# Optimization experiments

Hardware: AMD Instinct MI355X
Metric: run time of the kernel (lower is better)

## Reference

```python
import jax, jax.numpy as jnp
import numpy as np

ATT_DIM = 512
HEADS = 8
HEAD_DIM = ATT_DIM // HEADS
D_IN = 512
LEFT_MASK = 256
RIGHT_MASK = 0
LARGE = 1e30


def pos_encoding(S, d):
    # Transformer-XL sinusoid table over relative positions S-1 .. -(S-1), length 2S-1.
    inv_freq = (1.0 / (10000.0 ** (np.arange(0, d, 2.0) / d))).astype(np.float32)
    pos = jnp.arange(S - 1, -S, -1, dtype=jnp.float32)          # [2S-1]
    ang = pos[:, None] * jnp.asarray(inv_freq)[None, :]          # [2S-1, d/2]
    # concat([sin, cos], -1) on a trailing singleton -> interleaved sin/cos per frequency
    return jnp.stack([jnp.sin(ang), jnp.cos(ang)], axis=-1).reshape(2 * S - 1, d)


def rel_shift(x):
    # x: [B, N, S, 2S-1] -> [B, N, S, S] with out[i, j] = x[i, S-1 - i + j]
    B, N, S, L = x.shape
    x = jnp.pad(x, ((0, 0), (0, 0), (0, 0), (1, 0)))             # [B,N,S,L+1]
    x = x.reshape(B, N, L + 1, S)[:, :, 1:, :]                   # [B,N,L,S]
    x = x.reshape(B, N, S, L)
    return x[:, :, :, :S]


def setup_inputs() -> dict:
    key = jax.random.key(0)
    ks = jax.random.split(key, 9)
    B, S, D = 2, 2048, D_IN
    scale = 0.02
    return {
        "x": jax.random.normal(ks[0], (B, S, D), dtype=jnp.float32),
        "Wq": jax.random.normal(ks[1], (D, ATT_DIM), dtype=jnp.float32) * scale,
        "b_con": jax.random.normal(ks[2], (ATT_DIM,), dtype=jnp.float32) * scale,
        "b_rel": jax.random.normal(ks[3], (ATT_DIM,), dtype=jnp.float32) * scale,
        "Wk": jax.random.normal(ks[4], (D, ATT_DIM), dtype=jnp.float32) * scale,
        "Wkr": jax.random.normal(ks[5], (D_IN, ATT_DIM), dtype=jnp.float32) * scale,
        "Wv": jax.random.normal(ks[6], (D, ATT_DIM), dtype=jnp.float32) * scale,
        "bv": jax.random.normal(ks[7], (ATT_DIM,), dtype=jnp.float32) * scale,
        "x_len": jax.random.randint(ks[8], (B,), 1, S + 1).astype(jnp.int32),
    }


def reference(x, Wq, b_con, b_rel, Wk, Wkr, Wv, bv, x_len):
    B, S, D = x.shape
    N, Dh = HEADS, HEAD_DIM

    # content/relative query share the kernel (TiedDense) with separate biases
    q_lin = jnp.einsum('bsd,de->bse', x, Wq)
    q_con = (q_lin + b_con).reshape(B, S, N, Dh)
    q_rel = (q_lin + b_rel).reshape(B, S, N, Dh)
    k_con = jnp.einsum('bsd,de->bse', x, Wk).reshape(B, S, N, Dh)

    content_energy = jnp.einsum('bind,bjnd->bnij', q_con, k_con)  # [B,N,S,S]

    pos_emb = pos_encoding(S, D_IN)                               # [2S-1, D]
    k_rel = (pos_emb @ Wkr).reshape(2 * S - 1, N, Dh)
    relative_energy = jnp.einsum('bind,jnd->bnij', q_rel, k_rel)  # [B,N,S,2S-1]
    relative_energy = rel_shift(relative_energy)                  # [B,N,S,S]

    energy = (content_energy + relative_energy) / jnp.sqrt(jnp.float32(Dh))

    # sequence mask over keys (broadcast [B,1,1,S]) * banded mask (band_part)
    j = jnp.arange(S)
    seq_mask = (j[None, :] < x_len[:, None]).astype(jnp.float32)[:, None, None, :]
    i = jnp.arange(S)[:, None]
    band = ((i - j[None, :] <= LEFT_MASK) & (j[None, :] - i <= RIGHT_MASK)).astype(jnp.float32)
    mask = seq_mask * band[None, None, :, :]

    masked_energy = energy - (1.0 - mask) * LARGE
    attention = jax.nn.softmax(masked_energy, axis=-1)

    v = (jnp.einsum('bsd,de->bse', x, Wv) + bv).reshape(B, S, N, Dh)
    context = jnp.einsum('bnij,bjnd->bind', attention, v).reshape(B, S, N * Dh)
    return context
```

## Files before the change

### kernel.cpp

```cpp
#include <hip/hip_runtime.h>
#include <math.h>

#define S_ 2048
#define NH 8
#define CSL 320
#define LP 72

typedef __attribute__((ext_vector_type(8))) short short8;
typedef __attribute__((ext_vector_type(4))) float f32x4;
typedef unsigned short ushort_t;

__device__ __forceinline__ short bf16r(float x) {
    union { float f; unsigned u; } v; v.f = x;
    unsigned r = v.u + 0x7fffu + ((v.u >> 16) & 1u);
    return (short)(r >> 16);
}
__device__ __forceinline__ float b2f(ushort_t h) {
    union { float f; unsigned u; } v; v.u = ((unsigned)h) << 16; return v.f;
}

__global__ __launch_bounds__(256) void prep_kernel(
    const float* __restrict__ x,
    const float* __restrict__ Wq, const float* __restrict__ Wk,
    const float* __restrict__ Wv, const float* __restrict__ Wkr,
    ushort_t* __restrict__ WTq, ushort_t* __restrict__ WTk,
    ushort_t* __restrict__ WTv, ushort_t* __restrict__ WTkr,
    ushort_t* __restrict__ pos, ushort_t* __restrict__ xb16)
{
    const int widx = blockIdx.z;
    const int t = threadIdx.x;
    if (widx == 4) {
        const int base = blockIdx.y * 8 + blockIdx.x;
        const float C = -0.051905126482615036f;
        const int f = t;
#pragma unroll
        for (int rep = 0; rep < 6; ++rep) {
            const int r = base + rep * 64;
            unsigned pk = 0;
            if (r <= 256) {
                float ang = (float)r * exp2f(C * (float)f);
                unsigned s = (unsigned)(ushort_t)bf16r(sinf(ang));
                unsigned c = (unsigned)(ushort_t)bf16r(cosf(ang));
                pk = s | (c << 16);
            }
            ((unsigned*)pos)[(size_t)r * 256 + f] = pk;
        }
        return;
    }
    if (widx == 5) {
        const int sub = blockIdx.y * 8 + blockIdx.x;
        const size_t base = (size_t)sub * 32768;
#pragma unroll
        for (int it = 0; it < 8; ++it) {
            const size_t idx = base + (size_t)it * 4096 + (size_t)t * 16;
            const float* src = &x[idx];
            ushort_t t16[16];
#pragma unroll
            for (int u = 0; u < 16; ++u) t16[u] = (ushort_t)bf16r(src[u]);
            *(short8*)&xb16[idx]     = *(short8*)&t16[0];
            *(short8*)&xb16[idx + 8] = *(short8*)&t16[8];
        }
        return;
    }
    const float* W = (widx == 0) ? Wq : (widx == 1) ? Wk : (widx == 2) ? Wv : Wkr;
    ushort_t* WT   = (widx == 0) ? WTq : (widx == 1) ? WTk : (widx == 2) ? WTv : WTkr;
    const int k0 = blockIdx.x * 64, n0 = blockIdx.y * 64;
    __shared__ __align__(16) ushort_t T[64][72];
    const int srow = t >> 2, sc0 = (t & 3) * 16;
    const float* src = &W[(size_t)(k0 + srow) * 512 + n0 + sc0];
#pragma unroll
    for (int u = 0; u < 16; ++u) T[sc0 + u][srow] = (ushort_t)bf16r(src[u]);
    __syncthreads();
    ushort_t* dst = &WT[(size_t)(n0 + srow) * 512 + k0 + sc0];
    *(short8*)dst       = *(const short8*)&T[srow][sc0];
    *(short8*)(dst + 8) = *(const short8*)&T[srow][sc0 + 8];
}

__global__ __launch_bounds__(256) void qkv_gemm(
    const ushort_t* __restrict__ xb16,
    const ushort_t* __restrict__ WTq, const ushort_t* __restrict__ WTk,
    const ushort_t* __restrict__ WTv,
    const ushort_t* __restrict__ pos, const ushort_t* __restrict__ WTkr,
    const float* __restrict__ b_con, const float* __restrict__ b_rel,
    const float* __restrict__ bv, const int* __restrict__ xlen_p,
    ushort_t* __restrict__ qcon, ushort_t* __restrict__ qrel,
    ushort_t* __restrict__ kout, ushort_t* __restrict__ vT,
    ushort_t* __restrict__ krel)
{
    const int widx = blockIdx.y >> 3;
    const int tid = threadIdx.x, lane = tid & 63, w = tid >> 6;
    const int quad = lane >> 4, l16 = lane & 15;

    __shared__ __align__(16) ushort_t A_lds[2][128][40];
    __shared__ __align__(16) ushort_t B_lds[2][64][40];

    f32x4 acc[2][4];
#pragma unroll
    for (int mt = 0; mt < 2; ++mt)
#pragma unroll
        for (int nt = 0; nt < 4; ++nt) acc[mt][nt] = (f32x4){0.f, 0.f, 0.f, 0.f};

    const int arow = tid >> 1, ak0 = (tid & 1) * 16;
    const int brow = tid >> 2, bk0 = (tid & 3) * 8;

    const ushort_t* Asrc;
    const ushort_t* Bsrc;

    if (widx < 2) {
        const int m0 = blockIdx.x * 128;
        {
            const int xl = xlen_p[m0 >> 11];
            const int s0 = m0 & 2047;
            if (widx == 0) { if (s0 >= xl + 256) return; }
            else           { if (s0 >= xl + 63)  return; }
        }
        const int n0 = (blockIdx.y & 7) * 64;
        const ushort_t* WT = (widx == 0) ? WTq : WTk;
        Asrc = &xb16[(size_t)(m0 + arow) * 512 + ak0];
        Bsrc = &WT[(size_t)(n0 + brow) * 512 + bk0];
    } else if (widx == 2) {
        const int vb = (blockIdx.y & 7) * 32 + blockIdx.x;
        const int m0d = (vb & 3) * 128;
        const int n0j = (vb >> 2) * 64;
        Asrc = &WTv[(size_t)(m0d + arow) * 512 + ak0];
        Bsrc = &xb16[(size_t)(n0j + brow) * 512 + bk0];
    } else {
        if (blockIdx.x >= 24) return;
        const int m0 = (blockIdx.x >> 3) * 128;
        const int n0 = (blockIdx.x & 7) * 64;
        Asrc = &pos[(size_t)(m0 + arow) * 512 + ak0];
        Bsrc = &WTkr[(size_t)(n0 + brow) * 512 + bk0];
    }

    {
        short8 pa0 = *(const short8*)Asrc;
        short8 pa1 = *(const short8*)(Asrc + 8);
        short8 pb  = *(const short8*)Bsrc;
        *(short8*)&A_lds[0][arow][ak0]     = pa0;
        *(short8*)&A_lds[0][arow][ak0 + 8] = pa1;
        *(short8*)&B_lds[0][brow][bk0]     = pb;
        pa0 = *(const short8*)(Asrc + 32);
        pa1 = *(const short8*)(Asrc + 40);
        pb  = *(const short8*)(Bsrc + 32);
        __syncthreads();

#pragma unroll 1
        for (int it = 0; it < 16; ++it) {
            const int cur = it & 1;
            if (it < 15) {
                *(short8*)&A_lds[cur ^ 1][arow][ak0]     = pa0;
                *(short8*)&A_lds[cur ^ 1][arow][ak0 + 8] = pa1;
                *(short8*)&B_lds[cur ^ 1][brow][bk0]     = pb;
                if (it < 14) {
                    pa0 = *(const short8*)(Asrc + it * 32 + 64);
                    pa1 = *(const short8*)(Asrc + it * 32 + 72);
                    pb  = *(const short8*)(Bsrc + it * 32 + 64);
                }
            }
            short8 a0 = *(const short8*)&A_lds[cur][w * 32 + l16][quad * 8];
            short8 a1 = *(const short8*)&A_lds[cur][w * 32 + 16 + l16][quad * 8];
#pragma unroll
            for (int nt = 0; nt < 4; ++nt) {
                short8 bb = *(const short8*)&B_lds[cur][nt * 16 + l16][quad * 8];
                acc[0][nt] = __builtin_amdgcn_mfma_f32_16x16x32_bf16(a0, bb, acc[0][nt], 0, 0, 0);
                acc[1][nt] = __builtin_amdgcn_mfma_f32_16x16x32_bf16(a1, bb, acc[1][nt], 0, 0, 0);
            }
            __syncthreads();
        }
    }

    if (widx < 2) {
        const int m0 = blockIdx.x * 128;
        const int n0 = (blockIdx.y & 7) * 64;
#pragma unroll
        for (int nt = 0; nt < 4; ++nt) {
            const int col = n0 + nt * 16 + l16;
            float bc = 0.f, br = 0.f;
            if (widx == 0) { bc = b_con[col]; br = b_rel[col]; }
#pragma unroll
            for (int mt = 0; mt < 2; ++mt) {
#pragma unroll
                for (int reg = 0; reg < 4; ++reg) {
                    const size_t m = (size_t)(m0 + w * 32 + mt * 16 + quad * 4 + reg);
                    const float val = acc[mt][nt][reg];
                    if (widx == 0) {
                        qcon[m * 512 + col] = (ushort_t)bf16r((val + bc) * 0.125f);
                        qrel[m * 512 + col] = (ushort_t)bf16r((val + br) * 0.125f);
                    } else {
                        kout[m * 512 + col] = (ushort_t)bf16r(val);
                    }
                }
            }
        }
    } else if (widx == 2) {
        const int vb = (blockIdx.y & 7) * 32 + blockIdx.x;
        const int m0d = (vb & 3) * 128;
        const int n0j = (vb >> 2) * 64;
        const int b = n0j >> 11;
#pragma unroll
        for (int mt = 0; mt < 2; ++mt) {
#pragma unroll
            for (int reg = 0; reg < 4; ++reg) {
                const int d = m0d + w * 32 + mt * 16 + quad * 4 + reg;
                const int n = d >> 6, dd = d & 63;
                const float bvv = bv[d];
#pragma unroll
                for (int nt = 0; nt < 4; ++nt) {
                    const int s = (n0j + nt * 16 + l16) & 2047;
                    vT[((size_t)((b * NH + n) * 64 + dd)) * 2048 + s] =
                        (ushort_t)bf16r(acc[mt][nt][reg] + bvv);
                }
            }
        }
    } else {
        const int m0 = (blockIdx.x >> 3) * 128;
        const int n0 = (blockIdx.x & 7) * 64;
#pragma unroll
        for (int nt = 0; nt < 4; ++nt) {
            const int col = n0 + nt * 16 + l16;
#pragma unroll
            for (int mt = 0; mt < 2; ++mt)
#pragma unroll
                for (int reg = 0; reg < 4; ++reg) {
                    const size_t m = (size_t)(m0 + w * 32 + mt * 16 + quad * 4 + reg);
                    krel[m * 512 + col] = (ushort_t)bf16r(acc[mt][nt][reg]);
                }
        }
    }
}

__global__ __launch_bounds__(256) void rel_gemm(
    const ushort_t* __restrict__ qrel, const ushort_t* __restrict__ krel,
    const ushort_t* __restrict__ vT, const int* __restrict__ xlen_p,
    ushort_t* __restrict__ R3, float* __restrict__ vmean)
{
    const int tile = blockIdx.x, n = blockIdx.y, b = blockIdx.z;
    const int tid = threadIdx.x, lane = tid & 63, w = tid >> 6;
    const int quad = lane >> 4, l16 = lane & 15;

    __shared__ __align__(16) ushort_t A_lds[128][LP];
    __shared__ __align__(16) ushort_t B_lds[2][64][LP];

    if (tile == 16) {
        const int row = tid >> 2, seg = tid & 3;
        const ushort_t* src = &vT[((size_t)((b * NH + n) * 64 + row)) * 2048 + seg * 512];
        float sum = 0.f;
        for (int it = 0; it < 64; ++it) {
            short8 h = *(const short8*)(src + it * 8);
#pragma unroll
            for (int u = 0; u < 8; ++u) sum += b2f((ushort_t)h[u]);
        }
        float* scratch = (float*)A_lds;
        scratch[row * 4 + seg] = sum;
        __syncthreads();
        if (tid < 64) {
            float s = scratch[tid * 4] + scratch[tid * 4 + 1]
                    + scratch[tid * 4 + 2] + scratch[tid * 4 + 3];
            vmean[(size_t)b * 512 + n * 64 + tid] = s * (1.0f / (float)S_);
        }
        return;
    }

    const int i0 = tile * 128;
    if (i0 >= xlen_p[b] + 256) return;

    {
        const int srow = tid >> 1, sc0 = (tid & 1) * 32;
        const ushort_t* src = &qrel[((size_t)b * S_ + i0 + srow) * 512 + n * 64 + sc0];
#pragma unroll
        for (int u = 0; u < 4; ++u)
            *(short8*)&A_lds[srow][sc0 + u * 8] = *(const short8*)(src + u * 8);
    }

    const size_t rbase3 = (size_t)(b * NH + n) * S_ * CSL;
    const int srow2 = tid >> 2, sc2 = (tid & 3) * 16;

    short8 pb0, pb1;
    auto issueB = [&](int rc) {
        const ushort_t* src = &krel[(size_t)(rc * 64 + srow2) * 512 + n * 64 + sc2];
        pb0 = *(const short8*)src;
        pb1 = *(const short8*)(src + 8);
    };
    issueB(0);
    *(short8*)&B_lds[0][srow2][sc2]     = pb0;
    *(short8*)&B_lds[0][srow2][sc2 + 8] = pb1;
    issueB(1);
    __syncthreads();

#pragma unroll 1
    for (int rc = 0; rc < 5; ++rc) {
        const int cur = rc & 1;
        if (rc < 4) {
            *(short8*)&B_lds[cur ^ 1][srow2][sc2]     = pb0;
            *(short8*)&B_lds[cur ^ 1][srow2][sc2 + 8] = pb1;
            if (rc < 3) issueB(rc + 2);
        }

        short8 a[2][2];
#pragma unroll
        for (int mt = 0; mt < 2; ++mt) {
            a[mt][0] = *(const short8*)&A_lds[w * 32 + mt * 16 + l16][quad * 8];
            a[mt][1] = *(const short8*)&A_lds[w * 32 + mt * 16 + l16][quad * 8 + 32];
        }
#pragma unroll
        for (int nt = 0; nt < 4; ++nt) {
            short8 b0 = *(const short8*)&B_lds[cur][nt * 16 + l16][quad * 8];
            short8 b1 = *(const short8*)&B_lds[cur][nt * 16 + l16][quad * 8 + 32];
            const int r = rc * 64 + nt * 16 + l16;
#pragma unroll
            for (int mt = 0; mt < 2; ++mt) {
                f32x4 s = (f32x4){0.f, 0.f, 0.f, 0.f};
                s = __builtin_amdgcn_mfma_f32_16x16x32_bf16(a[mt][0], b0, s, 0, 0, 0);
                s = __builtin_amdgcn_mfma_f32_16x16x32_bf16(a[mt][1], b1, s, 0, 0, 0);
                if (r <= 256) {
#pragma unroll
                    for (int reg = 0; reg < 4; ++reg) {
                        const int ig = i0 + w * 32 + mt * 16 + quad * 4 + reg;
                        const int cslot = (ig & 63) + 256 - r;
                        R3[rbase3 + (size_t)ig * CSL + cslot] = (ushort_t)bf16r(s[reg]);
                    }
                }
            }
        }
        __syncthreads();
    }
}

__global__ __launch_bounds__(256) void attn_kernel(
    const ushort_t* __restrict__ qcon, const ushort_t* __restrict__ kbuf,
    const ushort_t* __restrict__ vT, const ushort_t* __restrict__ R3,
    const float* __restrict__ vmean, const int* __restrict__ xlen_p,
    float* __restrict__ out)
{
    const int bx = blockIdx.x;
    const int tile = ((bx & 7) << 2) | (bx >> 3);
    const int n = blockIdx.y, b = blockIdx.z;
    const int i0 = tile * 64;
    const int tid = threadIdx.x, lane = tid & 63, w = tid >> 6;
    const int quad = lane >> 4, l16 = lane & 15;
    const int xlen = xlen_p[b];

    if (i0 >= xlen + 256) {
        const int row = tid >> 2, cf = (tid & 3) * 16;
        const float* vm = &vmean[(size_t)b * 512 + n * 64 + cf];
        float* dst = &out[((size_t)b * S_ + i0 + row) * 512 + n * 64 + cf];
#pragma unroll
        for (int u = 0; u < 16; u += 4)
            *(float4*)&dst[u] = *(const float4*)&vm[u];
        return;
    }
    int nchunk = (xlen - i0 + 256 + 63) >> 6;
    if (nchunk > 5) nchunk = 5;
    const int c0 = (i0 < 256) ? ((256 - i0) >> 6) : 0;

    __shared__ __align__(16) ushort_t k_lds[64][LP];
    __shared__ __align__(16) ushort_t vT_lds[64][LP];
    __shared__ __align__(16) ushort_t Rl_lds[64][LP];

    const ushort_t* qc = &qcon[((size_t)b * S_ + i0 + w * 16 + l16) * 512 + n * 64 + quad * 8];
    const short8 aq0 = *(const short8*)qc;
    const short8 aq1 = *(const short8*)(qc + 32);

    f32x4 Oa[4];
#pragma unroll
    for (int nt = 0; nt < 4; ++nt) Oa[nt] = (f32x4){0.f, 0.f, 0.f, 0.f};
    float lpart[4] = {};

    const size_t rbase3 = (size_t)(b * NH + n) * S_ * CSL;
    const size_t vTbase = (size_t)((b * NH + n) * 64) * 2048;
    const int srow = tid >> 2, sc0 = (tid & 3) * 16;

    short8 kr[2], vr[2], rr[2], kn[2], vn[2], rn[2];

    auto issue = [&](int c, short8* kd, short8* vd, short8* rd) {
        const int jc0 = i0 - 256 + c * 64;
        const ushort_t* ks = &kbuf[((size_t)b * S_ + jc0 + srow) * 512 + n * 64 + sc0];
        kd[0] = *(const short8*)ks;
        kd[1] = *(const short8*)(ks + 8);
        const ushort_t* vs = &vT[vTbase + (size_t)srow * 2048 + jc0 + sc0];
        vd[0] = *(const short8*)vs;
        vd[1] = *(const short8*)(vs + 8);
        const ushort_t* Rs = &R3[rbase3 + (size_t)(i0 + srow) * CSL + c * 64 + sc0];
        rd[0] = *(const short8*)Rs;
        rd[1] = *(const short8*)(Rs + 8);
    };

    issue(c0, kr, vr, rr);

#pragma unroll 1
    for (int c = c0; c < nchunk; ++c) {
        const int jc0 = i0 - 256 + c * 64;
        __syncthreads();
        *(short8*)&k_lds[srow][sc0]      = kr[0];
        *(short8*)&k_lds[srow][sc0 + 8]  = kr[1];
        *(short8*)&vT_lds[srow][sc0]     = vr[0];
        *(short8*)&vT_lds[srow][sc0 + 8] = vr[1];
        *(short8*)&Rl_lds[srow][sc0]     = rr[0];
        *(short8*)&Rl_lds[srow][sc0 + 8] = rr[1];
        if (c + 1 < nchunk) issue(c + 1, kn, vn, rn);
        __syncthreads();

        f32x4 Sacc[4];
#pragma unroll
        for (int jt = 0; jt < 4; ++jt) {
            short8 bk0 = *(const short8*)&k_lds[jt * 16 + l16][quad * 8];
            short8 bk1 = *(const short8*)&k_lds[jt * 16 + l16][quad * 8 + 32];
            f32x4 s = (f32x4){0.f, 0.f, 0.f, 0.f};
            s = __builtin_amdgcn_mfma_f32_16x16x32_bf16(aq0, bk0, s, 0, 0, 0);
            s = __builtin_amdgcn_mfma_f32_16x16x32_bf16(aq1, bk1, s, 0, 0, 0);
            Sacc[jt] = s;
        }

#pragma unroll
        for (int jt = 0; jt < 4; ++jt) {
#pragma unroll
            for (int reg = 0; reg < 4; ++reg) {
                const int row = w * 16 + quad * 4 + reg;
                const int i = i0 + row;
                const int j = jc0 + jt * 16 + l16;
                const int r = i - j;
                const bool valid = (j < xlen) && (r >= 0) && (r <= 256);
                float rvv = b2f(Rl_lds[row][jt * 16 + l16]);
                float e = valid ? __expf(Sacc[jt][reg] + rvv) : 0.f;
                lpart[reg] += e;
                Rl_lds[row][jt * 16 + l16] = (ushort_t)bf16r(e);
            }
        }

        short8 ap0 = *(const short8*)&Rl_lds[w * 16 + l16][quad * 8];
        short8 ap1 = *(const short8*)&Rl_lds[w * 16 + l16][quad * 8 + 32];
#pragma unroll
        for (int nt = 0; nt < 4; ++nt) {
            short8 bv0 = *(const short8*)&vT_lds[nt * 16 + l16][quad * 8];
            short8 bv1 = *(const short8*)&vT_lds[nt * 16 + l16][quad * 8 + 32];
            Oa[nt] = __builtin_amdgcn_mfma_f32_16x16x32_bf16(ap0, bv0, Oa[nt], 0, 0, 0);
            Oa[nt] = __builtin_amdgcn_mfma_f32_16x16x32_bf16(ap1, bv1, Oa[nt], 0, 0, 0);
        }

        kr[0] = kn[0]; kr[1] = kn[1];
        vr[0] = vn[0]; vr[1] = vn[1];
        rr[0] = rn[0]; rr[1] = rn[1];
    }

#pragma unroll
    for (int reg = 0; reg < 4; ++reg) {
#pragma unroll
        for (int off = 1; off < 16; off <<= 1)
            lpart[reg] += __shfl_xor(lpart[reg], off, 64);
    }

#pragma unroll
    for (int reg = 0; reg < 4; ++reg) {
        const int i = i0 + w * 16 + quad * 4 + reg;
        const bool dead = (i >= xlen + 256);
        const float linv = 1.0f / lpart[reg];
#pragma unroll
        for (int nt = 0; nt < 4; ++nt) {
            const int d = n * 64 + nt * 16 + l16;
            float val = dead ? vmean[(size_t)b * 512 + d] : Oa[nt][reg] * linv;
            out[((size_t)b * S_ + i) * 512 + d] = val;
        }
    }
}

extern "C" void kernel_launch(void* const* d_in, const int* in_sizes, int n_in,
                              void* d_out, int out_size, void* d_ws, size_t ws_size,
                              hipStream_t stream) {
    const float* x     = (const float*)d_in[0];
    const float* Wq    = (const float*)d_in[1];
    const float* b_con = (const float*)d_in[2];
    const float* b_rel = (const float*)d_in[3];
    const float* Wk    = (const float*)d_in[4];
    const float* Wkr   = (const float*)d_in[5];
    const float* Wv    = (const float*)d_in[6];
    const float* bv    = (const float*)d_in[7];
    const int*   xlen  = (const int*)d_in[8];
    float* out = (float*)d_out;

    float* ws = (float*)d_ws;
    float* vmean = ws;
    ushort_t* ub   = (ushort_t*)(vmean + 1024);
    ushort_t* R3   = ub;
    ushort_t* qcon = R3   + 10485760;
    ushort_t* kbuf = qcon + 2097152;
    ushort_t* vT   = kbuf + 2097152;
    ushort_t* qrel = vT   + 2097152;
    ushort_t* xb16 = qrel + 2097152;
    ushort_t* krel = xb16 + 2097152;
    ushort_t* pos  = krel + 196608;
    ushort_t* WTq  = pos  + 196608;
    ushort_t* WTk  = WTq + 262144;
    ushort_t* WTv  = WTk + 262144;
    ushort_t* WTkr = WTv + 262144;

    prep_kernel<<<dim3(8, 8, 6), 256, 0, stream>>>(x, Wq, Wk, Wv, Wkr,
                                                   WTq, WTk, WTv, WTkr, pos, xb16);
    qkv_gemm<<<dim3(32, 25), 256, 0, stream>>>(xb16, WTq, WTk, WTv, pos, WTkr,
                                               b_con, b_rel, bv, xlen,
                                               qcon, qrel, kbuf, vT, krel);
    rel_gemm<<<dim3(17, 8, 2), 256, 0, stream>>>(qrel, krel, vT, xlen, R3, vmean);
    attn_kernel<<<dim3(32, 8, 2), 256, 0, stream>>>(qcon, kbuf, vT, R3, vmean,
                                                    xlen, out);
}
```

Before: 126.9 us.

## Fuse relative-position GEMM into attention kernel and compute vmean from x column sums

Removes the separate rel_gemm kernel and its large R3 global buffer. Each attention block now computes its relative-energy band (qrel × krel) directly into a widened shared-memory tile before the main loop. The value mean used for fully masked rows is now computed algebraically as mean(x)·Wv + bv. Column partial sums come from an extra prep slice and are reduced inside spare qkv_gemm blocks. This removes one launch and a large global write and read-back, at the cost of redundant krel loads per block and a much larger LDS footprint that may reduce occupancy.

```diff
diff --git a/kernel.cpp b/kernel.cpp
--- a/kernel.cpp
+++ b/kernel.cpp
@@ -3,8 +3,8 @@
 
 #define S_ 2048
 #define NH 8
-#define CSL 320
 #define LP 72
+#define RP 328
 
 typedef __attribute__((ext_vector_type(8))) short short8;
 typedef __attribute__((ext_vector_type(4))) float f32x4;
@@ -25,7 +25,8 @@
     const float* __restrict__ Wv, const float* __restrict__ Wkr,
     ushort_t* __restrict__ WTq, ushort_t* __restrict__ WTk,
     ushort_t* __restrict__ WTv, ushort_t* __restrict__ WTkr,
-    ushort_t* __restrict__ pos, ushort_t* __restrict__ xb16)
+    ushort_t* __restrict__ pos, ushort_t* __restrict__ xb16,
+    float* __restrict__ xpart)
 {
     const int widx = blockIdx.z;
     const int t = threadIdx.x;
@@ -62,6 +63,19 @@
         }
         return;
     }
+    if (widx == 6) {
+        const int sub = blockIdx.y * 8 + blockIdx.x;
+        const int b = sub >> 5, rb = sub & 31;
+        const float* src = &x[((size_t)b * 2048 + (size_t)rb * 64) * 512];
+        float s0 = 0.f, s1 = 0.f;
+        for (int r = 0; r < 64; ++r) {
+            s0 += src[(size_t)r * 512 + t];
+            s1 += src[(size_t)r * 512 + t + 256];
+        }
+        xpart[(size_t)sub * 512 + t]       = s0;
+        xpart[(size_t)sub * 512 + t + 256] = s1;
+        return;
+    }
     const float* W = (widx == 0) ? Wq : (widx == 1) ? Wk : (widx == 2) ? Wv : Wkr;
     ushort_t* WT   = (widx == 0) ? WTq : (widx == 1) ? WTk : (widx == 2) ? WTv : WTkr;
     const int k0 = blockIdx.x * 64, n0 = blockIdx.y * 64;
@@ -83,9 +97,10 @@
     const ushort_t* __restrict__ pos, const ushort_t* __restrict__ WTkr,
     const float* __restrict__ b_con, const float* __restrict__ b_rel,
     const float* __restrict__ bv, const int* __restrict__ xlen_p,
+    const float* __restrict__ xpart,
     ushort_t* __restrict__ qcon, ushort_t* __restrict__ qrel,
     ushort_t* __restrict__ kout, ushort_t* __restrict__ vT,
-    ushort_t* __restrict__ krel)
+    ushort_t* __restrict__ krel, float* __restrict__ vmean)
 {
     const int widx = blockIdx.y >> 3;
     const int tid = threadIdx.x, lane = tid & 63, w = tid >> 6;
@@ -125,7 +140,35 @@
         Asrc = &WTv[(size_t)(m0d + arow) * 512 + ak0];
         Bsrc = &xb16[(size_t)(n0j + brow) * 512 + bk0];
     } else {
-        if (blockIdx.x >= 24) return;
+        if (blockIdx.x >= 24) {
+            float* xm = (float*)A_lds;
+            for (int idx = tid; idx < 1024; idx += 256) {
+                const int bb = idx >> 9, k = idx & 511;
+                float s = 0.f;
+                for (int p = 0; p < 32; ++p)
+                    s += xpart[(size_t)(bb * 32 + p) * 512 + k];
+                xm[bb * 512 + k] = s * (1.0f / 2048.0f);
+            }
+            __syncthreads();
+            if (tid < 64) {
+                const int d = (blockIdx.x - 24) * 64 + tid;
+                const ushort_t* wrow = &WTv[(size_t)d * 512];
+                float a0 = 0.f, a1 = 0.f;
+                for (int k = 0; k < 512; k += 8) {
+                    short8 wv = *(const short8*)(wrow + k);
+#pragma unroll
+                    for (int u = 0; u < 8; ++u) {
+                        const float wf = b2f((ushort_t)wv[u]);
+                        a0 += xm[k + u] * wf;
+                        a1 += xm[512 + k + u] * wf;
+                    }
+                }
+                const float bvd = bv[d];
+                vmean[d]       = a0 + bvd;
+                vmean[512 + d] = a1 + bvd;
+            }
+            return;
+        }
         const int m0 = (blockIdx.x >> 3) * 128;
         const int n0 = (blockIdx.x & 7) * 64;
         Asrc = &pos[(size_t)(m0 + arow) * 512 + ak0];
@@ -229,108 +272,11 @@
     }
 }
 
-__global__ __launch_bounds__(256) void rel_gemm(
-    const ushort_t* __restrict__ qrel, const ushort_t* __restrict__ krel,
-    const ushort_t* __restrict__ vT, const int* __restrict__ xlen_p,
-    ushort_t* __restrict__ R3, float* __restrict__ vmean)
-{
-    const int tile = blockIdx.x, n = blockIdx.y, b = blockIdx.z;
-    const int tid = threadIdx.x, lane = tid & 63, w = tid >> 6;
-    const int quad = lane >> 4, l16 = lane & 15;
-
-    __shared__ __align__(16) ushort_t A_lds[128][LP];
-    __shared__ __align__(16) ushort_t B_lds[2][64][LP];
-
-    if (tile == 16) {
-        const int row = tid >> 2, seg = tid & 3;
-        const ushort_t* src = &vT[((size_t)((b * NH + n) * 64 + row)) * 2048 + seg * 512];
-        float sum = 0.f;
-        for (int it = 0; it < 64; ++it) {
-            short8 h = *(const short8*)(src + it * 8);
-#pragma unroll
-            for (int u = 0; u < 8; ++u) sum += b2f((ushort_t)h[u]);
-        }
-        float* scratch = (float*)A_lds;
-        scratch[row * 4 + seg] = sum;
-        __syncthreads();
-        if (tid < 64) {
-            float s = scratch[tid * 4] + scratch[tid * 4 + 1]
-                    + scratch[tid * 4 + 2] + scratch[tid * 4 + 3];
-            vmean[(size_t)b * 512 + n * 64 + tid] = s * (1.0f / (float)S_);
-        }
-        return;
-    }
-
-    const int i0 = tile * 128;
-    if (i0 >= xlen_p[b] + 256) return;
-
-    {
-        const int srow = tid >> 1, sc0 = (tid & 1) * 32;
-        const ushort_t* src = &qrel[((size_t)b * S_ + i0 + srow) * 512 + n * 64 + sc0];
-#pragma unroll
-        for (int u = 0; u < 4; ++u)
-            *(short8*)&A_lds[srow][sc0 + u * 8] = *(const short8*)(src + u * 8);
-    }
-
-    const size_t rbase3 = (size_t)(b * NH + n) * S_ * CSL;
-    const int srow2 = tid >> 2, sc2 = (tid & 3) * 16;
-
-    short8 pb0, pb1;
-    auto issueB = [&](int rc) {
-        const ushort_t* src = &krel[(size_t)(rc * 64 + srow2) * 512 + n * 64 + sc2];
-        pb0 = *(const short8*)src;
-        pb1 = *(const short8*)(src + 8);
-    };
-    issueB(0);
-    *(short8*)&B_lds[0][srow2][sc2]     = pb0;
-    *(short8*)&B_lds[0][srow2][sc2 + 8] = pb1;
-    issueB(1);
-    __syncthreads();
-
-#pragma unroll 1
-    for (int rc = 0; rc < 5; ++rc) {
-        const int cur = rc & 1;
-        if (rc < 4) {
-            *(short8*)&B_lds[cur ^ 1][srow2][sc2]     = pb0;
-            *(short8*)&B_lds[cur ^ 1][srow2][sc2 + 8] = pb1;
-            if (rc < 3) issueB(rc + 2);
-        }
-
-        short8 a[2][2];
-#pragma unroll
-        for (int mt = 0; mt < 2; ++mt) {
-            a[mt][0] = *(const short8*)&A_lds[w * 32 + mt * 16 + l16][quad * 8];
-            a[mt][1] = *(const short8*)&A_lds[w * 32 + mt * 16 + l16][quad * 8 + 32];
-        }
-#pragma unroll
-        for (int nt = 0; nt < 4; ++nt) {
-            short8 b0 = *(const short8*)&B_lds[cur][nt * 16 + l16][quad * 8];
-            short8 b1 = *(const short8*)&B_lds[cur][nt * 16 + l16][quad * 8 + 32];
-            const int r = rc * 64 + nt * 16 + l16;
-#pragma unroll
-            for (int mt = 0; mt < 2; ++mt) {
-                f32x4 s = (f32x4){0.f, 0.f, 0.f, 0.f};
-                s = __builtin_amdgcn_mfma_f32_16x16x32_bf16(a[mt][0], b0, s, 0, 0, 0);
-                s = __builtin_amdgcn_mfma_f32_16x16x32_bf16(a[mt][1], b1, s, 0, 0, 0);
-                if (r <= 256) {
-#pragma unroll
-                    for (int reg = 0; reg < 4; ++reg) {
-                        const int ig = i0 + w * 32 + mt * 16 + quad * 4 + reg;
-                        const int cslot = (ig & 63) + 256 - r;
-                        R3[rbase3 + (size_t)ig * CSL + cslot] = (ushort_t)bf16r(s[reg]);
-                    }
-                }
-            }
-        }
-        __syncthreads();
-    }
-}
-
 __global__ __launch_bounds__(256) void attn_kernel(
-    const ushort_t* __restrict__ qcon, const ushort_t* __restrict__ kbuf,
-    const ushort_t* __restrict__ vT, const ushort_t* __restrict__ R3,
-    const float* __restrict__ vmean, const int* __restrict__ xlen_p,
-    float* __restrict__ out)
+    const ushort_t* __restrict__ qcon, const ushort_t* __restrict__ qrel,
+    const ushort_t* __restrict__ kbuf, const ushort_t* __restrict__ vT,
+    const ushort_t* __restrict__ krel, const float* __restrict__ vmean,
+    const int* __restrict__ xlen_p, float* __restrict__ out)
 {
     const int bx = blockIdx.x;
     const int tile = ((bx & 7) << 2) | (bx >> 3);
@@ -355,7 +301,42 @@
 
     __shared__ __align__(16) ushort_t k_lds[64][LP];
     __shared__ __align__(16) ushort_t vT_lds[64][LP];
-    __shared__ __align__(16) ushort_t Rl_lds[64][LP];
+    __shared__ __align__(16) ushort_t R_lds[64][RP];
+
+    const int srow = tid >> 2, sc0 = (tid & 3) * 16;
+
+    {
+        const ushort_t* qr = &qrel[((size_t)b * S_ + i0 + w * 16 + l16) * 512 + n * 64 + quad * 8];
+        const short8 ar0 = *(const short8*)qr;
+        const short8 ar1 = *(const short8*)(qr + 32);
+        const int rlim = (i0 + 63 < 256) ? i0 + 63 : 256;
+#pragma unroll 1
+        for (int rc = 0; rc <= (rlim >> 6); ++rc) {
+            const ushort_t* ks = &krel[(size_t)(rc * 64 + srow) * 512 + n * 64 + sc0];
+            short8 s0v = *(const short8*)ks;
+            short8 s1v = *(const short8*)(ks + 8);
+            __syncthreads();
+            *(short8*)&k_lds[srow][sc0]     = s0v;
+            *(short8*)&k_lds[srow][sc0 + 8] = s1v;
+            __syncthreads();
+#pragma unroll
+            for (int nt = 0; nt < 4; ++nt) {
+                if (rc * 64 + nt * 16 <= rlim) {
+                    short8 b0 = *(const short8*)&k_lds[nt * 16 + l16][quad * 8];
+                    short8 b1 = *(const short8*)&k_lds[nt * 16 + l16][quad * 8 + 32];
+                    f32x4 s = (f32x4){0.f, 0.f, 0.f, 0.f};
+                    s = __builtin_amdgcn_mfma_f32_16x16x32_bf16(ar0, b0, s, 0, 0, 0);
+                    s = __builtin_amdgcn_mfma_f32_16x16x32_bf16(ar1, b1, s, 0, 0, 0);
+                    const int r = rc * 64 + nt * 16 + l16;
+#pragma unroll
+                    for (int reg = 0; reg < 4; ++reg) {
+                        const int rowq = w * 16 + quad * 4 + reg;
+                        if (r <= 256) R_lds[rowq][rowq + 256 - r] = (ushort_t)bf16r(s[reg]);
+                    }
+                }
+            }
+        }
+    }
 
     const ushort_t* qc = &qcon[((size_t)b * S_ + i0 + w * 16 + l16) * 512 + n * 64 + quad * 8];
     const short8 aq0 = *(const short8*)qc;
@@ -366,13 +347,11 @@
     for (int nt = 0; nt < 4; ++nt) Oa[nt] = (f32x4){0.f, 0.f, 0.f, 0.f};
     float lpart[4] = {};
 
-    const size_t rbase3 = (size_t)(b * NH + n) * S_ * CSL;
     const size_t vTbase = (size_t)((b * NH + n) * 64) * 2048;
-    const int srow = tid >> 2, sc0 = (tid & 3) * 16;
-
-    short8 kr[2], vr[2], rr[2], kn[2], vn[2], rn[2];
-
-    auto issue = [&](int c, short8* kd, short8* vd, short8* rd) {
+
+    short8 kr[2], vr[2], kn[2], vn[2];
+
+    auto issue = [&](int c, short8* kd, short8* vd) {
         const int jc0 = i0 - 256 + c * 64;
         const ushort_t* ks = &kbuf[((size_t)b * S_ + jc0 + srow) * 512 + n * 64 + sc0];
         kd[0] = *(const short8*)ks;
@@ -380,12 +359,9 @@
         const ushort_t* vs = &vT[vTbase + (size_t)srow * 2048 + jc0 + sc0];
         vd[0] = *(const short8*)vs;
         vd[1] = *(const short8*)(vs + 8);
-        const ushort_t* Rs = &R3[rbase3 + (size_t)(i0 + srow) * CSL + c * 64 + sc0];
-        rd[0] = *(const short8*)Rs;
-        rd[1] = *(const short8*)(Rs + 8);
     };
 
-    issue(c0, kr, vr, rr);
+    issue(c0, kr, vr);
 
 #pragma unroll 1
     for (int c = c0; c < nchunk; ++c) {
@@ -395,9 +371,7 @@
         *(short8*)&k_lds[srow][sc0 + 8]  = kr[1];
         *(short8*)&vT_lds[srow][sc0]     = vr[0];
         *(short8*)&vT_lds[srow][sc0 + 8] = vr[1];
-        *(short8*)&Rl_lds[srow][sc0]     = rr[0];
-        *(short8*)&Rl_lds[srow][sc0 + 8] = rr[1];
-        if (c + 1 < nchunk) issue(c + 1, kn, vn, rn);
+        if (c + 1 < nchunk) issue(c + 1, kn, vn);
         __syncthreads();
 
         f32x4 Sacc[4];
@@ -420,15 +394,15 @@
                 const int j = jc0 + jt * 16 + l16;
                 const int r = i - j;
                 const bool valid = (j < xlen) && (r >= 0) && (r <= 256);
-                float rvv = b2f(Rl_lds[row][jt * 16 + l16]);
+                float rvv = b2f(R_lds[row][c * 64 + jt * 16 + l16]);
                 float e = valid ? __expf(Sacc[jt][reg] + rvv) : 0.f;
                 lpart[reg] += e;
-                Rl_lds[row][jt * 16 + l16] = (ushort_t)bf16r(e);
-            }
-        }
-
-        short8 ap0 = *(const short8*)&Rl_lds[w * 16 + l16][quad * 8];
-        short8 ap1 = *(const short8*)&Rl_lds[w * 16 + l16][quad * 8 + 32];
+                R_lds[row][c * 64 + jt * 16 + l16] = (ushort_t)bf16r(e);
+            }
+        }
+
+        short8 ap0 = *(const short8*)&R_lds[w * 16 + l16][c * 64 + quad * 8];
+        short8 ap1 = *(const short8*)&R_lds[w * 16 + l16][c * 64 + quad * 8 + 32];
 #pragma unroll
         for (int nt = 0; nt < 4; ++nt) {
             short8 bv0 = *(const short8*)&vT_lds[nt * 16 + l16][quad * 8];
@@ -439,7 +413,6 @@
 
         kr[0] = kn[0]; kr[1] = kn[1];
         vr[0] = vn[0]; vr[1] = vn[1];
-        rr[0] = rn[0]; rr[1] = rn[1];
     }
 
 #pragma unroll
@@ -479,9 +452,9 @@
 
     float* ws = (float*)d_ws;
     float* vmean = ws;
-    ushort_t* ub   = (ushort_t*)(vmean + 1024);
-    ushort_t* R3   = ub;
-    ushort_t* qcon = R3   + 10485760;
+    float* xpart = vmean + 1024;
+    ushort_t* ub   = (ushort_t*)(xpart + 32768);
+    ushort_t* qcon = ub;
     ushort_t* kbuf = qcon + 2097152;
     ushort_t* vT   = kbuf + 2097152;
     ushort_t* qrel = vT   + 2097152;
@@ -493,12 +466,12 @@
     ushort_t* WTv  = WTk + 262144;
     ushort_t* WTkr = WTv + 262144;
 
-    prep_kernel<<<dim3(8, 8, 6), 256, 0, stream>>>(x, Wq, Wk, Wv, Wkr,
-                                                   WTq, WTk, WTv, WTkr, pos, xb16);
+    prep_kernel<<<dim3(8, 8, 7), 256, 0, stream>>>(x, Wq, Wk, Wv, Wkr,
+                                                   WTq, WTk, WTv, WTkr, pos, xb16,
+                                                   xpart);
     qkv_gemm<<<dim3(32, 25), 256, 0, stream>>>(xb16, WTq, WTk, WTv, pos, WTkr,
-                                               b_con, b_rel, bv, xlen,
-                                               qcon, qrel, kbuf, vT, krel);
-    rel_gemm<<<dim3(17, 8, 2), 256, 0, stream>>>(qrel, krel, vT, xlen, R3, vmean);
-    attn_kernel<<<dim3(32, 8, 2), 256, 0, stream>>>(qcon, kbuf, vT, R3, vmean,
-                                                    xlen, out);
-}
+                                               b_con, b_rel, bv, xlen, xpart,
+                                               qcon, qrel, kbuf, vT, krel, vmean);
+    attn_kernel<<<dim3(32, 8, 2), 256, 0, stream>>>(qcon, qrel, kbuf, vT, krel,
+                                                    vmean, xlen, out);
+}
```

After: 124.2 us. 2.1% less time.
